# Kernel tuning notes

Hardware: AMD Instinct MI355X
Metric: run time of the kernel (lower is better)

The kernel has to match this reference:

```python
import jax, jax.numpy as jnp
import numpy as np

N_NODES = 50000
N_EDGES = 200000
D_IN = 512
D_OUT = 512

def setup_inputs() -> dict:
    key = jax.random.key(0)
    k1, k2, k3, k4, k5, k6 = jax.random.split(key, 6)
    h = jax.random.normal(k1, (N_NODES, D_IN), dtype=jnp.float32)
    W = jax.random.normal(k2, (D_IN, D_OUT), dtype=jnp.float32) * (1.0 / np.sqrt(D_IN))
    b = jax.random.normal(k3, (D_OUT,), dtype=jnp.float32) * 0.01
    edge_weight = jax.random.uniform(k4, (N_EDGES,), dtype=jnp.float32)
    src = jax.random.randint(k5, (N_EDGES,), 0, N_NODES, dtype=jnp.int32)
    dst = jax.random.randint(k6, (N_EDGES,), 0, N_NODES, dtype=jnp.int32)
    return {"h": h, "W": W, "b": b, "edge_weight": edge_weight, "src": src, "dst": dst}

def reference(h, W, b, edge_weight, src, dst):
    # Linear projection of source-node features (nn.Linear)
    h_proj = h @ W + b                                   # [N, D_OUT]
    # u_mul_e: gather projected src features, scale by scalar edge weight
    msg = h_proj[src] * edge_weight[:, None]             # [E, D_OUT]
    # mean aggregation over incoming edges per destination node (DGL fn.mean)
    sums = jax.ops.segment_sum(msg, dst, num_segments=N_NODES)          # [N, D_OUT]
    cnt = jax.ops.segment_sum(jnp.ones_like(edge_weight), dst, num_segments=N_NODES)  # [N]
    agg = sums / jnp.maximum(cnt, 1.0)[:, None]          # zero-in-degree nodes -> 0
    # ReLU then dropout (eval mode -> identity)
    return jax.nn.relu(agg)
```

## Files before the change

### kernel.cpp

```cpp
#include <hip/hip_runtime.h>

#define NNODES 50000
#define NEDGES 200000
#define DDIM 512

typedef __attribute__((ext_vector_type(8))) short bf16x8;
typedef __attribute__((ext_vector_type(4))) float f32x4;

static __device__ __forceinline__ unsigned short f2bf(float f) {
  unsigned u = __float_as_uint(f);
  unsigned r = (u + 0x7fffu + ((u >> 16) & 1u)) >> 16;
  return (unsigned short)r;
}

static __device__ __forceinline__ void gload_lds16(const void* g, void* l) {
  __builtin_amdgcn_global_load_lds(
      (const __attribute__((address_space(1))) unsigned int*)g,
      (__attribute__((address_space(3))) unsigned int*)l, 16, 0, 0);
}

__global__ __launch_bounds__(256) void cvt_h_kernel(
    const float* __restrict__ in, unsigned short* __restrict__ out, int n8) {
  for (int i = blockIdx.x * 256 + threadIdx.x; i < n8; i += gridDim.x * 256) {
    const float4 v0 = ((const float4*)in)[(size_t)i * 2];
    const float4 v1 = ((const float4*)in)[(size_t)i * 2 + 1];
    uint4 p;
    p.x = (unsigned)f2bf(v0.x) | ((unsigned)f2bf(v0.y) << 16);
    p.y = (unsigned)f2bf(v0.z) | ((unsigned)f2bf(v0.w) << 16);
    p.z = (unsigned)f2bf(v1.x) | ((unsigned)f2bf(v1.y) << 16);
    p.w = (unsigned)f2bf(v1.z) | ((unsigned)f2bf(v1.w) << 16);
    ((uint4*)out)[i] = p;
  }
}

__global__ __launch_bounds__(256) void cvt_wt_kernel(
    const float* __restrict__ W, unsigned short* __restrict__ Wt,
    int* __restrict__ deg) {
  const int gid = (blockIdx.x + blockIdx.y * gridDim.x) * 256 + threadIdx.x;
  if (gid < NNODES) deg[gid] = 0;

  __shared__ float t[32][33];
  const int n0 = blockIdx.x * 32, k0 = blockIdx.y * 32;
  const int tx = threadIdx.x & 31, ty = threadIdx.x >> 5;
  for (int r = ty; r < 32; r += 8)
    t[r][tx] = W[(size_t)(k0 + r) * DDIM + n0 + tx];
  __syncthreads();
  for (int r = ty; r < 32; r += 8)
    Wt[(size_t)(n0 + r) * DDIM + k0 + tx] = f2bf(t[tx][r]);
}

__global__ __launch_bounds__(256) void gemm_mfma_kernel(
    const unsigned short* __restrict__ Ab, const unsigned short* __restrict__ Bt,
    const float* __restrict__ bias, unsigned short* __restrict__ C, int M) {
  __shared__ unsigned short As[2][128 * 32];
  __shared__ unsigned short Bs[2][128 * 32];
  const int tid = threadIdx.x;
  const int wid = tid >> 6, lane = tid & 63;

  const int nwg = gridDim.x;
  const int q = nwg >> 3, rr = nwg & 7;
  const int x = blockIdx.x & 7, idx = blockIdx.x >> 3;
  const int wg = x * q + min(x, rr) + idx;

  const int mt = wg >> 2, nt = wg & 3;
  const int bm = mt * 128, bn = nt * 128;
  const int wr = wid >> 1, wc = wid & 1;

  f32x4 acc[4][4] = {};

  const int r0 = tid >> 2;
  const int cge = (tid & 3) ^ ((r0 >> 1) & 3);

  const int arow0 = min(bm + r0, M - 1);
  const int arow1 = min(bm + r0 + 64, M - 1);

  const unsigned short* a0 = Ab + (size_t)arow0 * DDIM + cge * 8;
  const unsigned short* a1 = Ab + (size_t)arow1 * DDIM + cge * 8;
  const unsigned short* b0 = Bt + (size_t)(bn + r0) * DDIM + cge * 8;
  const unsigned short* b1 = Bt + (size_t)(bn + r0 + 64) * DDIM + cge * 8;

  const int l16 = lane & 15, lk = lane >> 4;
  const int lke = lk ^ ((l16 >> 1) & 3);

  const int sOff0 = (wid * 64) * 8;
  const int sOff1 = (256 + wid * 64) * 8;

#define STAGE(buf, k0)                        \
  do {                                        \
    gload_lds16(a0 + (k0), &As[buf][sOff0]);  \
    gload_lds16(a1 + (k0), &As[buf][sOff1]);  \
    gload_lds16(b0 + (k0), &Bs[buf][sOff0]);  \
    gload_lds16(b1 + (k0), &Bs[buf][sOff1]);  \
  } while (0)

#define COMPUTE(buf)                                                          \
  do {                                                                        \
    bf16x8 af[4], bfr[4];                                                     \
    _Pragma("unroll") for (int i = 0; i < 4; ++i) {                           \
      af[i]  = *(const bf16x8*)&As[buf][(wr * 64 + i * 16 + l16) * 32 + lke * 8]; \
      bfr[i] = *(const bf16x8*)&Bs[buf][(wc * 64 + i * 16 + l16) * 32 + lke * 8]; \
    }                                                                         \
    _Pragma("unroll") for (int i = 0; i < 4; ++i)                             \
        _Pragma("unroll") for (int j = 0; j < 4; ++j)                         \
            acc[i][j] = __builtin_amdgcn_mfma_f32_16x16x32_bf16(              \
                af[i], bfr[j], acc[i][j], 0, 0, 0);                           \
  } while (0)

  STAGE(0, 0);
  __syncthreads();
#pragma unroll 2
  for (int t = 0; t < 15; ++t) {
    const int cur = t & 1;
    STAGE(cur ^ 1, (t + 1) * 32);
    COMPUTE(cur);
    __syncthreads();
  }
  COMPUTE(1);
  __syncthreads();

  unsigned short* cl = (wid < 2) ? &As[0][0] + wid * 4096
                                 : &Bs[0][0] + (wid - 2) * 4096;
#pragma unroll
  for (int j = 0; j < 4; ++j) {
    const float bv = bias[bn + wc * 64 + j * 16 + l16];
#pragma unroll
    for (int i = 0; i < 4; ++i)
#pragma unroll
      for (int qq = 0; qq < 4; ++qq)
        cl[(i * 16 + lk * 4 + qq) * 64 + j * 16 + l16] =
            f2bf(acc[i][j][qq] + bv);
  }
  __syncthreads();
#pragma unroll
  for (int pass = 0; pass < 8; ++pass) {
    const int rt = pass * 8 + (lane >> 3);
    const int c0 = (lane & 7) * 8;
    const int grow = bm + wr * 64 + rt;
    if (grow < M) {
      const uint4 v = *(const uint4*)&cl[rt * 64 + c0];
      *(uint4*)&C[(size_t)grow * DDIM + bn + wc * 64 + c0] = v;
    }
  }
#undef STAGE
#undef COMPUTE
}

__global__ __launch_bounds__(256) void hist_kernel(const int* __restrict__ dst,
                                                   int* __restrict__ deg, int E) {
  const int e = blockIdx.x * 256 + threadIdx.x;
  if (e < E) atomicAdd(&deg[dst[e]], 1);
}

__global__ __launch_bounds__(256) void chunk_sum_kernel(
    const int* __restrict__ deg, int* __restrict__ part, int n) {
  const int base = blockIdx.x * 1024;
  int v = 0;
  for (int i = threadIdx.x; i < 1024; i += 256) {
    const int idx = base + i;
    v += (idx < n) ? deg[idx] : 0;
  }
#pragma unroll
  for (int s = 32; s; s >>= 1) v += __shfl_down(v, s, 64);
  __shared__ int ws[4];
  if ((threadIdx.x & 63) == 0) ws[threadIdx.x >> 6] = v;
  __syncthreads();
  if (threadIdx.x == 0) part[blockIdx.x] = ws[0] + ws[1] + ws[2] + ws[3];
}

__global__ void scan_part_kernel(int* __restrict__ part, int nb) {
  const int lane = threadIdx.x & 63;
  int v = (lane < nb) ? part[lane] : 0;
  int incl = v;
#pragma unroll
  for (int s = 1; s < 64; s <<= 1) {
    int t = __shfl_up(incl, s, 64);
    if (lane >= s) incl += t;
  }
  if (lane < nb) part[lane] = incl - v;
}

__global__ __launch_bounds__(1024) void chunk_scan_kernel(
    const int* __restrict__ deg, const int* __restrict__ part,
    int* __restrict__ off, int* __restrict__ cur, int n) {
  __shared__ int wsum[16];
  const int tid = threadIdx.x, lane = tid & 63, wid = tid >> 6;
  const int i = blockIdx.x * 1024 + tid;
  const int v = (i < n) ? deg[i] : 0;
  int incl = v;
#pragma unroll
  for (int s = 1; s < 64; s <<= 1) {
    int t = __shfl_up(incl, s, 64);
    if (lane >= s) incl += t;
  }
  if (lane == 63) wsum[wid] = incl;
  __syncthreads();
  if (wid == 0 && lane < 16) {
    int wv = wsum[lane];
#pragma unroll
    for (int s = 1; s < 16; s <<= 1) {
      int t = __shfl_up(wv, s, 16);
      if (lane >= s) wv += t;
    }
    wsum[lane] = wv;
  }
  __syncthreads();
  const int add = part[blockIdx.x] + ((wid > 0) ? wsum[wid - 1] : 0);
  if (i < n) {
    off[i + 1] = add + incl;
    cur[i] = add + incl - v;
  }
  if (i == 0) off[0] = 0;
}

__global__ __launch_bounds__(256) void fill_kernel(
    const int* __restrict__ src, const int* __restrict__ dst,
    const float* __restrict__ ew, int* __restrict__ cur,
    uint2* __restrict__ epair, int E) {
  const int e = blockIdx.x * 256 + threadIdx.x;
  if (e >= E) return;
  const int p = atomicAdd(&cur[dst[e]], 1);
  epair[p] = make_uint2((unsigned)src[e], __float_as_uint(ew[e]));
}

__global__ __launch_bounds__(256) void gather_kernel(
    const unsigned short* __restrict__ hp, const int* __restrict__ off,
    const uint2* __restrict__ epair, float* __restrict__ out, int n) {
  const int node = blockIdx.x * 4 + (threadIdx.x >> 6);
  if (node >= n) return;
  const int lane = threadIdx.x & 63;
  const int beg = off[node], end = off[node + 1];

  float acc[8] = {0.f, 0.f, 0.f, 0.f, 0.f, 0.f, 0.f, 0.f};
  int p = beg;
  for (; p + 2 <= end; p += 2) {
    const uint2 e0 = epair[p];
    const uint2 e1 = epair[p + 1];
    const float w0 = __uint_as_float(e0.y);
    const float w1 = __uint_as_float(e1.y);
    const uint4 u0 = *(const uint4*)(hp + (size_t)e0.x * DDIM + lane * 8);
    const uint4 u1 = *(const uint4*)(hp + (size_t)e1.x * DDIM + lane * 8);
    const unsigned a0[4] = {u0.x, u0.y, u0.z, u0.w};
    const unsigned a1[4] = {u1.x, u1.y, u1.z, u1.w};
#pragma unroll
    for (int qv = 0; qv < 4; ++qv) {
      acc[2 * qv + 0] += w0 * __uint_as_float(a0[qv] << 16) +
                         w1 * __uint_as_float(a1[qv] << 16);
      acc[2 * qv + 1] += w0 * __uint_as_float(a0[qv] & 0xffff0000u) +
                         w1 * __uint_as_float(a1[qv] & 0xffff0000u);
    }
  }
  if (p < end) {
    const uint2 e0 = epair[p];
    const float w0 = __uint_as_float(e0.y);
    const uint4 u0 = *(const uint4*)(hp + (size_t)e0.x * DDIM + lane * 8);
    const unsigned a0[4] = {u0.x, u0.y, u0.z, u0.w};
#pragma unroll
    for (int qv = 0; qv < 4; ++qv) {
      acc[2 * qv + 0] += w0 * __uint_as_float(a0[qv] << 16);
      acc[2 * qv + 1] += w0 * __uint_as_float(a0[qv] & 0xffff0000u);
    }
  }

  const float inv = 1.0f / fmaxf((float)(end - beg), 1.0f);
  f32x4 o0, o1;
  o0.x = fmaxf(acc[0] * inv, 0.f);
  o0.y = fmaxf(acc[1] * inv, 0.f);
  o0.z = fmaxf(acc[2] * inv, 0.f);
  o0.w = fmaxf(acc[3] * inv, 0.f);
  o1.x = fmaxf(acc[4] * inv, 0.f);
  o1.y = fmaxf(acc[5] * inv, 0.f);
  o1.z = fmaxf(acc[6] * inv, 0.f);
  o1.w = fmaxf(acc[7] * inv, 0.f);
  float* orow = out + (size_t)node * DDIM + lane * 8;
  __builtin_nontemporal_store(o0, (f32x4*)(orow + 0));
  __builtin_nontemporal_store(o1, (f32x4*)(orow + 4));
}

extern "C" void kernel_launch(void* const* d_in, const int* in_sizes, int n_in,
                              void* d_out, int out_size, void* d_ws, size_t ws_size,
                              hipStream_t stream) {
  const float* h  = (const float*)d_in[0];
  const float* W  = (const float*)d_in[1];
  const float* b  = (const float*)d_in[2];
  const float* ew = (const float*)d_in[3];
  const int* src  = (const int*)d_in[4];
  const int* dst  = (const int*)d_in[5];
  float* out = (float*)d_out;

  unsigned short* hb = (unsigned short*)d_out;
  unsigned short* Wt = (unsigned short*)((char*)d_out + (size_t)NNODES * DDIM * 2);

  char* ws = (char*)d_ws;
  size_t o = 0;
  auto alloc = [&](size_t bytes) {
    char* p = ws + o;
    o += (bytes + 255) & ~(size_t)255;
    return p;
  };
  unsigned short* hp = (unsigned short*)alloc((size_t)NNODES * DDIM * 2);
  int* deg    = (int*)alloc((size_t)NNODES * 4);
  int* off    = (int*)alloc((size_t)(NNODES + 1) * 4);
  int* cur    = (int*)alloc((size_t)NNODES * 4);
  uint2* epair = (uint2*)alloc((size_t)NEDGES * 8);
  int* part   = (int*)alloc(64 * 4);

  const int nchunks = (NNODES + 1023) / 1024;

  cvt_h_kernel<<<2048, 256, 0, stream>>>(h, hb, NNODES * DDIM / 8);
  dim3 wgrid(16, 16);
  cvt_wt_kernel<<<wgrid, 256, 0, stream>>>(W, Wt, deg);

  const int mtiles = (NNODES + 127) / 128;
  gemm_mfma_kernel<<<mtiles * 4, 256, 0, stream>>>(hb, Wt, b, hp, NNODES);

  hist_kernel<<<(NEDGES + 255) / 256, 256, 0, stream>>>(dst, deg, NEDGES);
  chunk_sum_kernel<<<nchunks, 256, 0, stream>>>(deg, part, NNODES);
  scan_part_kernel<<<1, 64, 0, stream>>>(part, nchunks);
  chunk_scan_kernel<<<nchunks, 1024, 0, stream>>>(deg, part, off, cur, NNODES);
  fill_kernel<<<(NEDGES + 255) / 256, 256, 0, stream>>>(src, dst, ew, cur,
                                                        epair, NEDGES);

  gather_kernel<<<(NNODES + 3) / 4, 256, 0, stream>>>(hp, off, epair, out,
                                                      NNODES);
}
```

Baseline: 151.2 us.

## Fuse fp32-to-bf16 conversion of h into GEMM A-tile loads

Removes the separate cvt_h pass that wrote a bf16 copy of h. The GEMM now streams fp32 h straight into LDS with a swizzled layout and converts each fragment to bf16 with v_cvt_pk_bf16_f32 before the MFMA. This saves a full read and write of h, but each of the 4 N-tile blocks now reads fp32 A, which doubles the A bytes per block and adds conversion work and LDS traffic inside the inner loop. Wt also moves into the workspace instead of the output buffer.

```diff
diff --git a/kernel.cpp b/kernel.cpp
--- a/kernel.cpp
+++ b/kernel.cpp
@@ -19,18 +19,13 @@
       (__attribute__((address_space(3))) unsigned int*)l, 16, 0, 0);
 }
 
-__global__ __launch_bounds__(256) void cvt_h_kernel(
-    const float* __restrict__ in, unsigned short* __restrict__ out, int n8) {
-  for (int i = blockIdx.x * 256 + threadIdx.x; i < n8; i += gridDim.x * 256) {
-    const float4 v0 = ((const float4*)in)[(size_t)i * 2];
-    const float4 v1 = ((const float4*)in)[(size_t)i * 2 + 1];
-    uint4 p;
-    p.x = (unsigned)f2bf(v0.x) | ((unsigned)f2bf(v0.y) << 16);
-    p.y = (unsigned)f2bf(v0.z) | ((unsigned)f2bf(v0.w) << 16);
-    p.z = (unsigned)f2bf(v1.x) | ((unsigned)f2bf(v1.y) << 16);
-    p.w = (unsigned)f2bf(v1.z) | ((unsigned)f2bf(v1.w) << 16);
-    ((uint4*)out)[i] = p;
-  }
+static __device__ __forceinline__ bf16x8 cvt_frag(f32x4 lo, f32x4 hi) {
+  union { bf16x8 v; unsigned u[4]; } r;
+  asm("v_cvt_pk_bf16_f32 %0, %1, %2" : "=v"(r.u[0]) : "v"(lo.x), "v"(lo.y));
+  asm("v_cvt_pk_bf16_f32 %0, %1, %2" : "=v"(r.u[1]) : "v"(lo.z), "v"(lo.w));
+  asm("v_cvt_pk_bf16_f32 %0, %1, %2" : "=v"(r.u[2]) : "v"(hi.x), "v"(hi.y));
+  asm("v_cvt_pk_bf16_f32 %0, %1, %2" : "=v"(r.u[3]) : "v"(hi.z), "v"(hi.w));
+  return r.v;
 }
 
 __global__ __launch_bounds__(256) void cvt_wt_kernel(
@@ -50,9 +45,9 @@
 }
 
 __global__ __launch_bounds__(256) void gemm_mfma_kernel(
-    const unsigned short* __restrict__ Ab, const unsigned short* __restrict__ Bt,
+    const float* __restrict__ A, const unsigned short* __restrict__ Bt,
     const float* __restrict__ bias, unsigned short* __restrict__ C, int M) {
-  __shared__ unsigned short As[2][128 * 32];
+  __shared__ float Af[2][128 * 32];
   __shared__ unsigned short Bs[2][128 * 32];
   const int tid = threadIdx.x;
   const int wid = tid >> 6, lane = tid & 63;
@@ -68,36 +63,47 @@
 
   f32x4 acc[4][4] = {};
 
+  const int lr = lane >> 3;
+  const int kqs = (lane & 7) ^ lr;
+  const int ar0 = min(bm + 0 * 32 + wid * 8 + lr, M - 1);
+  const int ar1 = min(bm + 1 * 32 + wid * 8 + lr, M - 1);
+  const int ar2 = min(bm + 2 * 32 + wid * 8 + lr, M - 1);
+  const int ar3 = min(bm + 3 * 32 + wid * 8 + lr, M - 1);
+  const float* pa0 = A + (size_t)ar0 * DDIM + kqs * 4;
+  const float* pa1 = A + (size_t)ar1 * DDIM + kqs * 4;
+  const float* pa2 = A + (size_t)ar2 * DDIM + kqs * 4;
+  const float* pa3 = A + (size_t)ar3 * DDIM + kqs * 4;
+
   const int r0 = tid >> 2;
   const int cge = (tid & 3) ^ ((r0 >> 1) & 3);
-
-  const int arow0 = min(bm + r0, M - 1);
-  const int arow1 = min(bm + r0 + 64, M - 1);
-
-  const unsigned short* a0 = Ab + (size_t)arow0 * DDIM + cge * 8;
-  const unsigned short* a1 = Ab + (size_t)arow1 * DDIM + cge * 8;
   const unsigned short* b0 = Bt + (size_t)(bn + r0) * DDIM + cge * 8;
   const unsigned short* b1 = Bt + (size_t)(bn + r0 + 64) * DDIM + cge * 8;
 
   const int l16 = lane & 15, lk = lane >> 4;
   const int lke = lk ^ ((l16 >> 1) & 3);
+  const int s7 = l16 & 7;
 
   const int sOff0 = (wid * 64) * 8;
   const int sOff1 = (256 + wid * 64) * 8;
 
-#define STAGE(buf, k0)                        \
-  do {                                        \
-    gload_lds16(a0 + (k0), &As[buf][sOff0]);  \
-    gload_lds16(a1 + (k0), &As[buf][sOff1]);  \
-    gload_lds16(b0 + (k0), &Bs[buf][sOff0]);  \
-    gload_lds16(b1 + (k0), &Bs[buf][sOff1]);  \
+#define STAGE(buf, k0)                                   \
+  do {                                                   \
+    gload_lds16(pa0 + (k0), &Af[buf][wid * 256]);        \
+    gload_lds16(pa1 + (k0), &Af[buf][1024 + wid * 256]); \
+    gload_lds16(pa2 + (k0), &Af[buf][2048 + wid * 256]); \
+    gload_lds16(pa3 + (k0), &Af[buf][3072 + wid * 256]); \
+    gload_lds16(b0 + (k0), &Bs[buf][sOff0]);             \
+    gload_lds16(b1 + (k0), &Bs[buf][sOff1]);             \
   } while (0)
 
 #define COMPUTE(buf)                                                          \
   do {                                                                        \
     bf16x8 af[4], bfr[4];                                                     \
     _Pragma("unroll") for (int i = 0; i < 4; ++i) {                           \
-      af[i]  = *(const bf16x8*)&As[buf][(wr * 64 + i * 16 + l16) * 32 + lke * 8]; \
+      const int rowi = (wr * 64 + i * 16 + l16) * 32;                         \
+      const f32x4 lo = *(const f32x4*)&Af[buf][rowi + (((2 * lk) ^ s7) << 2)];\
+      const f32x4 hi = *(const f32x4*)&Af[buf][rowi + (((2 * lk + 1) ^ s7) << 2)]; \
+      af[i] = cvt_frag(lo, hi);                                               \
       bfr[i] = *(const bf16x8*)&Bs[buf][(wc * 64 + i * 16 + l16) * 32 + lke * 8]; \
     }                                                                         \
     _Pragma("unroll") for (int i = 0; i < 4; ++i)                             \
@@ -118,8 +124,7 @@
   COMPUTE(1);
   __syncthreads();
 
-  unsigned short* cl = (wid < 2) ? &As[0][0] + wid * 4096
-                                 : &Bs[0][0] + (wid - 2) * 4096;
+  unsigned short* cl = (unsigned short*)&Af[0][0] + wid * 4096;
 #pragma unroll
   for (int j = 0; j < 4; ++j) {
     const float bv = bias[bn + wc * 64 + j * 16 + l16];
@@ -287,9 +292,6 @@
   const int* dst  = (const int*)d_in[5];
   float* out = (float*)d_out;
 
-  unsigned short* hb = (unsigned short*)d_out;
-  unsigned short* Wt = (unsigned short*)((char*)d_out + (size_t)NNODES * DDIM * 2);
-
   char* ws = (char*)d_ws;
   size_t o = 0;
   auto alloc = [&](size_t bytes) {
@@ -298,6 +300,7 @@
     return p;
   };
   unsigned short* hp = (unsigned short*)alloc((size_t)NNODES * DDIM * 2);
+  unsigned short* Wt = (unsigned short*)alloc((size_t)DDIM * DDIM * 2);
   int* deg    = (int*)alloc((size_t)NNODES * 4);
   int* off    = (int*)alloc((size_t)(NNODES + 1) * 4);
   int* cur    = (int*)alloc((size_t)NNODES * 4);
@@ -306,12 +309,11 @@
 
   const int nchunks = (NNODES + 1023) / 1024;
 
-  cvt_h_kernel<<<2048, 256, 0, stream>>>(h, hb, NNODES * DDIM / 8);
   dim3 wgrid(16, 16);
   cvt_wt_kernel<<<wgrid, 256, 0, stream>>>(W, Wt, deg);
 
   const int mtiles = (NNODES + 127) / 128;
-  gemm_mfma_kernel<<<mtiles * 4, 256, 0, stream>>>(hb, Wt, b, hp, NNODES);
+  gemm_mfma_kernel<<<mtiles * 4, 256, 0, stream>>>(h, Wt, b, hp, NNODES);
 
   hist_kernel<<<(NEDGES + 255) / 256, 256, 0, stream>>>(dst, deg, NEDGES);
   chunk_sum_kernel<<<nchunks, 256, 0, stream>>>(deg, part, NNODES);
```

Result: faster. 138.0 us (-8.7%).
